# Performance work log

Hardware: AMD Instinct MI355X
Metric: run time of the kernel (lower is better)

The kernel has to match this reference:

```python
import jax, jax.numpy as jnp
import numpy as np

DIM = 256
HEADS = 8
HEAD_DIM = DIM // HEADS
SCALE = HEAD_DIM ** -0.5
EPS_LN = 1e-5
EPS_NORM = 1e-12


def setup_inputs() -> dict:
    key = jax.random.key(0)
    ks = jax.random.split(key, 12)
    B, C, H, W = 8, DIM, 32, 32
    s = 0.02
    return {
        "x": jax.random.normal(ks[0], (B, C, H, W), jnp.float32),
        "dw_w": jax.random.normal(ks[1], (C, 1, 3, 3), jnp.float32) * s,
        "dw_b": jnp.zeros((C,), jnp.float32),
        "qkv_w": jax.random.normal(ks[2], (3 * C, C), jnp.float32) * s,
        "c1_w": jax.random.normal(ks[3], (C, C), jnp.float32) * s,
        "c1_b": jnp.zeros((C,), jnp.float32),
        "ln1_g": jnp.ones((C,), jnp.float32),
        "ln1_b": jnp.zeros((C,), jnp.float32),
        "c2_w": jax.random.normal(ks[4], (C, C), jnp.float32) * s,
        "c2_b": jnp.zeros((C,), jnp.float32),
        "ln2_g": jnp.ones((C,), jnp.float32),
        "ln2_b": jnp.zeros((C,), jnp.float32),
    }


def _l2norm(t):
    n = jnp.sqrt(jnp.sum(t * t, axis=-1, keepdims=True))
    return t / jnp.maximum(n, EPS_NORM)


def _layernorm_c(x_nchw, g, b):
    # LayerNorm over channel dim of an NCHW tensor (torch does permute->LN->permute)
    mu = jnp.mean(x_nchw, axis=1, keepdims=True)
    var = jnp.mean((x_nchw - mu) ** 2, axis=1, keepdims=True)
    xn = (x_nchw - mu) * jax.lax.rsqrt(var + EPS_LN)
    return xn * g[None, :, None, None] + b[None, :, None, None]


def _gelu(x):
    return jax.nn.gelu(x, approximate=False)


def reference(x, dw_w, dw_b, qkv_w, c1_w, c1_b, ln1_g, ln1_b, c2_w, c2_b, ln2_g, ln2_b):
    B, C, H, W = x.shape
    identity = x
    # depthwise 3x3 conv
    y = jax.lax.conv_general_dilated(
        x, dw_w, window_strides=(1, 1), padding="SAME",
        dimension_numbers=("NCHW", "OIHW", "NCHW"), feature_group_count=C)
    y = y + dw_b[None, :, None, None]
    # tokens [B, N, C]
    t = y.reshape(B, C, H * W).transpose(0, 2, 1)
    qkv = jnp.einsum("bnc,oc->bno", t, qkv_w)  # [B,N,3C]
    qkv = qkv.reshape(B, H * W, 3, HEADS, HEAD_DIM).transpose(2, 0, 3, 1, 4)
    q, k, v = qkv[0], qkv[1], qkv[2]  # [B,h,N,d]
    q = _l2norm(q)
    k = _l2norm(k)
    attn = jnp.einsum("bhnd,bhmd->bhnm", q, k) * SCALE
    attn = jax.nn.softmax(attn, axis=-1)
    o = jnp.einsum("bhnm,bhmd->bhnd", attn, v)  # [B,h,N,d]
    o = o.transpose(0, 2, 1, 3).reshape(B, H * W, C)
    y = o.transpose(0, 2, 1).reshape(B, C, H, W)
    # conv-MLP branch (1x1 convs as channel GEMMs)
    y = jnp.einsum("bchw,oc->bohw", y, c1_w) + c1_b[None, :, None, None]
    y = _gelu(_layernorm_c(y, ln1_g, ln1_b))
    y = jnp.einsum("bchw,oc->bohw", y, c2_w) + c2_b[None, :, None, None]
    y = _gelu(_layernorm_c(y, ln2_g, ln2_b))
    return identity + y
```

## Files before the change

kernel.cpp:

```cpp
#include <hip/hip_runtime.h>
#include <math.h>

#define DIMC 256
#define NTOK 1024
#define QKVN 768
#define HDIM 32

typedef __attribute__((ext_vector_type(8))) short bf16x8;
typedef __attribute__((ext_vector_type(4))) float f32x4;
typedef __attribute__((ext_vector_type(4))) unsigned short us4;

__device__ __forceinline__ unsigned short f2bf(float f) {
  unsigned u = __float_as_uint(f);
  u += 0x7FFF + ((u >> 16) & 1);
  return (unsigned short)(u >> 16);
}

__device__ __forceinline__ float gelu_f(float y) {
  return 0.5f * y * (1.f + erff(y * 0.70710678118654752f));
}

__global__ void dwconv_k(const float* __restrict__ x, const float* __restrict__ w,
                         const float* __restrict__ b, float* __restrict__ y) {
  int bc = blockIdx.x;
  int c = bc & (DIMC - 1);
  float wr[9];
#pragma unroll
  for (int i = 0; i < 9; i++) wr[i] = w[c * 9 + i];
  float bb = b[c];
  const float* xp = x + (size_t)bc * NTOK;
  float* yp = y + (size_t)bc * NTOK;
  for (int p = threadIdx.x; p < NTOK; p += 256) {
    int hh = p >> 5, ww = p & 31;
    float acc = bb;
#pragma unroll
    for (int dh = 0; dh < 3; dh++) {
      int h2 = hh + dh - 1;
      if ((unsigned)h2 < 32u) {
#pragma unroll
        for (int dw = 0; dw < 3; dw++) {
          int w2 = ww + dw - 1;
          if ((unsigned)w2 < 32u) acc += xp[h2 * 32 + w2] * wr[dh * 3 + dw];
        }
      }
    }
    yp[p] = acc;
  }
}

__global__ void cvt_w_k(const float* __restrict__ w0, const float* __restrict__ w1,
                        const float* __restrict__ w2, unsigned short* __restrict__ Wb) {
  int i = (blockIdx.x * 256 + threadIdx.x) * 4;
  const float* src;
  int off;
  if (i < 196608) { src = w0; off = i; }
  else if (i < 262144) { src = w1; off = i - 196608; }
  else { src = w2; off = i - 262144; }
  float4 v = *(const float4*)(src + off);
  us4 o = {f2bf(v.x), f2bf(v.y), f2bf(v.z), f2bf(v.w)};
  *(us4*)(Wb + i) = o;
}

__global__ void t2b_k(const float* __restrict__ y2, unsigned short* __restrict__ A0) {
  __shared__ float tile[32][33];
  int b = blockIdx.z, c0 = blockIdx.y << 5, s0 = blockIdx.x << 5;
  int t = threadIdx.x;
  int j = t & 31, i0 = t >> 5;
#pragma unroll
  for (int i = i0; i < 32; i += 8)
    tile[i][j] = y2[(size_t)(b * 256 + c0 + i) * 1024 + s0 + j];
  __syncthreads();
#pragma unroll
  for (int i2 = i0; i2 < 32; i2 += 8)
    A0[(size_t)(b * 1024 + s0 + i2) * 256 + c0 + j] = f2bf(tile[j][i2]);
}

template <bool BIAS>
__global__ __launch_bounds__(256) void mgemm_k(const unsigned short* __restrict__ A,
                                               const unsigned short* __restrict__ W,
                                               const float* __restrict__ bias,
                                               float* __restrict__ C, int N) {
  __shared__ __align__(16) unsigned short As[128 * 40];
  __shared__ __align__(16) unsigned short Bs[64 * 40];
  const int t = threadIdx.x;
  const int m0 = blockIdx.y * 128;
  const int n0 = blockIdx.x * 64;
  const int wid = t >> 6, lane = t & 63;
  const int lg = lane >> 4, lr = lane & 15;
  const int wm0 = (wid >> 1) * 64, wn0 = (wid & 1) * 32;

  f32x4 acc[4][2] = {};
  for (int k0 = 0; k0 < 256; k0 += 32) {
    __syncthreads();
    {
#pragma unroll
      for (int u = 0; u < 2; u++) {
        int f = t + u * 256;
        int r = f >> 2, c = f & 3;
        bf16x8 v = *(const bf16x8*)(A + (size_t)(m0 + r) * 256 + k0 + c * 8);
        *(bf16x8*)&As[r * 40 + c * 8] = v;
      }
      int o = t >> 2, c = t & 3;
      bf16x8 v = *(const bf16x8*)(W + (size_t)(n0 + o) * 256 + k0 + c * 8);
      *(bf16x8*)&Bs[o * 40 + c * 8] = v;
    }
    __syncthreads();
    bf16x8 af[4], bfr[2];
#pragma unroll
    for (int mt = 0; mt < 4; mt++)
      af[mt] = *(const bf16x8*)&As[(wm0 + mt * 16 + lr) * 40 + lg * 8];
#pragma unroll
    for (int nt = 0; nt < 2; nt++)
      bfr[nt] = *(const bf16x8*)&Bs[(wn0 + nt * 16 + lr) * 40 + lg * 8];
#pragma unroll
    for (int mt = 0; mt < 4; mt++)
#pragma unroll
      for (int nt = 0; nt < 2; nt++)
        acc[mt][nt] = __builtin_amdgcn_mfma_f32_16x16x32_bf16(af[mt], bfr[nt], acc[mt][nt], 0, 0, 0);
  }
  float bv[2];
#pragma unroll
  for (int nt = 0; nt < 2; nt++)
    bv[nt] = BIAS ? bias[n0 + wn0 + nt * 16 + lr] : 0.f;
#pragma unroll
  for (int mt = 0; mt < 4; mt++)
#pragma unroll
    for (int nt = 0; nt < 2; nt++)
#pragma unroll
      for (int r = 0; r < 4; r++) {
        int row = m0 + wm0 + mt * 16 + lg * 4 + r;
        int col = n0 + wn0 + nt * 16 + lr;
        C[(size_t)row * N + col] = acc[mt][nt][r] + bv[nt];
      }
}

__global__ void cvt_qkv_k(const float* __restrict__ qkv,
                          unsigned short* __restrict__ Qb,
                          unsigned short* __restrict__ Kb,
                          unsigned short* __restrict__ Vb) {
  int n = blockIdx.x;
  int t = threadIdx.x;
  int b = n >> 10, nr = n & 1023;
  int sec = t >> 6, lane = t & 63;
  if (sec < 2) {
    const float* p = qkv + (size_t)n * QKVN + sec * 256 + lane * 4;
    float4 v = *(const float4*)p;
    float s = v.x * v.x + v.y * v.y + v.z * v.z + v.w * v.w;
    s += __shfl_xor(s, 1, 64); s += __shfl_xor(s, 2, 64); s += __shfl_xor(s, 4, 64);
    float inv = 1.f / fmaxf(sqrtf(s), 1e-12f);
    if (sec == 0) inv *= 0.17677669529663687f;
    int h = lane >> 3, d4 = (lane & 7) << 2;
    unsigned short* dst = (sec == 0 ? Qb : Kb) + ((size_t)((b * 8 + h) * 1024 + nr)) * 32 + d4;
    us4 o = {f2bf(v.x * inv), f2bf(v.y * inv), f2bf(v.z * inv), f2bf(v.w * inv)};
    *(us4*)dst = o;
  } else {
    int i = t - 128;
    const float* p = qkv + (size_t)n * QKVN + 512 + i * 2;
    float2 v = *(const float2*)p;
    int c = i * 2;
    int h = c >> 5, d = c & 31;
    unsigned short* dst = Vb + ((size_t)((b * 8 + h) * 1024 + nr)) * 32 + d;
    ushort2 o = {f2bf(v.x), f2bf(v.y)};
    *(ushort2*)dst = o;
  }
}

#define PSTR 56

__global__ __launch_bounds__(128) void attn_mfma_k(const unsigned short* __restrict__ Qb,
                                                   const unsigned short* __restrict__ Kb,
                                                   const unsigned short* __restrict__ Vb,
                                                   unsigned short* __restrict__ obuf) {
  __shared__ unsigned short Vt[32 * PSTR];
  __shared__ unsigned short Pl[2][32 * PSTR];
  const int bh = blockIdx.y;
  const int chunk = blockIdx.x;
  const int tid = threadIdx.x;
  const int wid = tid >> 6, lane = tid & 63;
  const int lg = lane >> 4, lr = lane & 15;
  const int q0 = chunk * 64 + wid * 32;
  const size_t base = (size_t)bh * NTOK;

  bf16x8 qf[2];
#pragma unroll
  for (int qt = 0; qt < 2; qt++)
    qf[qt] = *(const bf16x8*)(Qb + (base + q0 + qt * 16 + lr) * 32 + lg * 8);

  f32x4 o[2][2] = {};
  float lpart[2][4] = {};

  for (int step = 0; step < 32; step++) {
    const int kv0 = step * 32;
    __syncthreads();
    {
      int kv = tid >> 2, d0 = (tid & 3) * 8;
      bf16x8 v = *(const bf16x8*)(Vb + (base + kv0 + kv) * 32 + d0);
#pragma unroll
      for (int i = 0; i < 8; i++) Vt[(d0 + i) * PSTR + kv] = (unsigned short)v[i];
    }
    __syncthreads();
    bf16x8 kf[2];
#pragma unroll
    for (int ct = 0; ct < 2; ct++)
      kf[ct] = *(const bf16x8*)(Kb + (base + kv0 + ct * 16 + lr) * 32 + lg * 8);
    unsigned short* pw = &Pl[wid][0];
#pragma unroll
    for (int qt = 0; qt < 2; qt++) {
#pragma unroll
      for (int ct = 0; ct < 2; ct++) {
        f32x4 c = {};
        c = __builtin_amdgcn_mfma_f32_16x16x32_bf16(qf[qt], kf[ct], c, 0, 0, 0);
#pragma unroll
        for (int r = 0; r < 4; r++) {
          float p = __expf(c[r]);
          lpart[qt][r] += p;
          pw[(qt * 16 + lg * 4 + r) * PSTR + ct * 16 + lr] = f2bf(p);
        }
      }
    }
#pragma unroll
    for (int qt = 0; qt < 2; qt++) {
      bf16x8 pf = *(const bf16x8*)(pw + (qt * 16 + lr) * PSTR + lg * 8);
#pragma unroll
      for (int dt = 0; dt < 2; dt++) {
        bf16x8 vf = *(const bf16x8*)(&Vt[(dt * 16 + lr) * PSTR + lg * 8]);
        o[qt][dt] = __builtin_amdgcn_mfma_f32_16x16x32_bf16(pf, vf, o[qt][dt], 0, 0, 0);
      }
    }
  }
#pragma unroll
  for (int qt = 0; qt < 2; qt++) {
#pragma unroll
    for (int r = 0; r < 4; r++) {
      float l = lpart[qt][r];
      l += __shfl_xor(l, 1, 64); l += __shfl_xor(l, 2, 64);
      l += __shfl_xor(l, 4, 64); l += __shfl_xor(l, 8, 64);
      lpart[qt][r] = 1.f / l;
    }
  }
  const int b = bh >> 3, h = bh & 7;
#pragma unroll
  for (int qt = 0; qt < 2; qt++)
#pragma unroll
    for (int dt = 0; dt < 2; dt++)
#pragma unroll
      for (int r = 0; r < 4; r++) {
        int q = q0 + qt * 16 + lg * 4 + r;
        int c = h * 32 + dt * 16 + lr;
        obuf[((size_t)(b * NTOK + q)) * DIMC + c] = f2bf(o[qt][dt][r] * lpart[qt][r]);
      }
}

template <bool OBF>
__global__ void ln_gelu_k(const float* __restrict__ in, const float* __restrict__ g,
                          const float* __restrict__ bb, void* __restrict__ outv) {
  int t = threadIdx.x;
  int lane = t & 63;
  int r = blockIdx.x * 4 + (t >> 6);
  const float* p = in + ((size_t)r << 8) + (lane << 2);
  float4 v = *(const float4*)p;
  float s1 = v.x + v.y + v.z + v.w;
  float s2 = v.x * v.x + v.y * v.y + v.z * v.z + v.w * v.w;
#pragma unroll
  for (int m = 1; m < 64; m <<= 1) {
    s1 += __shfl_xor(s1, m, 64);
    s2 += __shfl_xor(s2, m, 64);
  }
  float mu = s1 * (1.f / 256.f);
  float var = s2 * (1.f / 256.f) - mu * mu;
  float rstd = rsqrtf(var + 1e-5f);
  float4 gv = *(const float4*)(g + (lane << 2));
  float4 bv = *(const float4*)(bb + (lane << 2));
  float4 ov;
  ov.x = gelu_f((v.x - mu) * rstd * gv.x + bv.x);
  ov.y = gelu_f((v.y - mu) * rstd * gv.y + bv.y);
  ov.z = gelu_f((v.z - mu) * rstd * gv.z + bv.z);
  ov.w = gelu_f((v.w - mu) * rstd * gv.w + bv.w);
  if (OBF) {
    us4 ob = {f2bf(ov.x), f2bf(ov.y), f2bf(ov.z), f2bf(ov.w)};
    *(us4*)((unsigned short*)outv + ((size_t)r << 8) + (lane << 2)) = ob;
  } else {
    *(float4*)((float*)outv + ((size_t)r << 8) + (lane << 2)) = ov;
  }
}

__global__ void trans_add_k(const float* __restrict__ m2, const float* __restrict__ x,
                            float* __restrict__ out) {
  __shared__ float tile[32][33];
  int b = blockIdx.z, c0 = blockIdx.y << 5, s0 = blockIdx.x << 5;
  int t = threadIdx.x;
  int j = t & 31, i0 = t >> 5;
#pragma unroll
  for (int i = i0; i < 32; i += 8)
    tile[i][j] = m2[(size_t)(b * 1024 + s0 + i) * 256 + c0 + j];
  __syncthreads();
#pragma unroll
  for (int i2 = i0; i2 < 32; i2 += 8) {
    size_t idx = ((size_t)(b * 256 + c0 + i2) << 10) + s0 + j;
    out[idx] = x[idx] + tile[j][i2];
  }
}

extern "C" void kernel_launch(void* const* d_in, const int* in_sizes, int n_in,
                              void* d_out, int out_size, void* d_ws, size_t ws_size,
                              hipStream_t stream) {
  const float* x     = (const float*)d_in[0];
  const float* dw_w  = (const float*)d_in[1];
  const float* dw_b  = (const float*)d_in[2];
  const float* qkv_w = (const float*)d_in[3];
  const float* c1_w  = (const float*)d_in[4];
  const float* c1_b  = (const float*)d_in[5];
  const float* ln1_g = (const float*)d_in[6];
  const float* ln1_b = (const float*)d_in[7];
  const float* c2_w  = (const float*)d_in[8];
  const float* c2_b  = (const float*)d_in[9];
  const float* ln2_g = (const float*)d_in[10];
  const float* ln2_b = (const float*)d_in[11];
  float* out = (float*)d_out;

  float* ws = (float*)d_ws;
  const size_t MF = (size_t)1 << 20;
  float* y2   = ws;
  unsigned short* A0 = (unsigned short*)(ws + 2 * MF);
  unsigned short* Wb = (unsigned short*)(ws + 3 * MF);
  float* qkv  = ws + 4 * MF;
  unsigned short* Qb = (unsigned short*)(ws + 10 * MF);
  unsigned short* Kb = (unsigned short*)(ws + 11 * MF);
  unsigned short* Vb = (unsigned short*)(ws + 12 * MF);
  unsigned short* obuf = (unsigned short*)ws;
  unsigned short* m1 = (unsigned short*)(ws + 1 * MF);
  float* buf1 = ws + 4 * MF;
  float* buf2 = ws + 6 * MF;
  float* m2b  = ws + 8 * MF;
  (void)in_sizes; (void)n_in; (void)out_size; (void)ws_size;

  dwconv_k<<<2048, 256, 0, stream>>>(x, dw_w, dw_b, y2);
  cvt_w_k<<<320, 256, 0, stream>>>(qkv_w, c1_w, c2_w, Wb);
  t2b_k<<<dim3(32, 8, 8), 256, 0, stream>>>(y2, A0);
  mgemm_k<false><<<dim3(12, 64), 256, 0, stream>>>(A0, Wb, nullptr, qkv, 768);
  cvt_qkv_k<<<8192, 256, 0, stream>>>(qkv, Qb, Kb, Vb);
  attn_mfma_k<<<dim3(16, 64), 128, 0, stream>>>(Qb, Kb, Vb, obuf);
  mgemm_k<true><<<dim3(4, 64), 256, 0, stream>>>(obuf, Wb + 196608, c1_b, buf1, 256);
  ln_gelu_k<true><<<2048, 256, 0, stream>>>(buf1, ln1_g, ln1_b, m1);
  mgemm_k<true><<<dim3(4, 64), 256, 0, stream>>>(m1, Wb + 262144, c2_b, buf2, 256);
  ln_gelu_k<false><<<2048, 256, 0, stream>>>(buf2, ln2_g, ln2_b, m2b);
  trans_add_k<<<dim3(32, 8, 8), 256, 0, stream>>>(m2b, x, out);
}
```

Baseline: 185.2 us.

## Pre-transpose V in a separate kernel and drop per-step LDS transpose in attention

Adds a kernel that writes V in a per-head transposed [d][token] bf16 layout, so the attention kernel reads V fragments straight from global memory instead of transposing into shared memory each step. The attention kernel shrinks to a single wave per block with no __syncthreads, which doubles the grid, and the P staging buffer gets a tighter stride. This removes the block barriers and LDS transpose work, but it adds one kernel launch and makes V reads uncached global accesses repeated across every query block.

```diff
diff --git a/kernel.cpp b/kernel.cpp
--- a/kernel.cpp
+++ b/kernel.cpp
@@ -136,50 +136,64 @@
 
 __global__ void cvt_qkv_k(const float* __restrict__ qkv,
                           unsigned short* __restrict__ Qb,
-                          unsigned short* __restrict__ Kb,
-                          unsigned short* __restrict__ Vb) {
+                          unsigned short* __restrict__ Kb) {
   int n = blockIdx.x;
   int t = threadIdx.x;
   int b = n >> 10, nr = n & 1023;
   int sec = t >> 6, lane = t & 63;
-  if (sec < 2) {
-    const float* p = qkv + (size_t)n * QKVN + sec * 256 + lane * 4;
-    float4 v = *(const float4*)p;
-    float s = v.x * v.x + v.y * v.y + v.z * v.z + v.w * v.w;
-    s += __shfl_xor(s, 1, 64); s += __shfl_xor(s, 2, 64); s += __shfl_xor(s, 4, 64);
-    float inv = 1.f / fmaxf(sqrtf(s), 1e-12f);
-    if (sec == 0) inv *= 0.17677669529663687f;
-    int h = lane >> 3, d4 = (lane & 7) << 2;
-    unsigned short* dst = (sec == 0 ? Qb : Kb) + ((size_t)((b * 8 + h) * 1024 + nr)) * 32 + d4;
-    us4 o = {f2bf(v.x * inv), f2bf(v.y * inv), f2bf(v.z * inv), f2bf(v.w * inv)};
-    *(us4*)dst = o;
-  } else {
-    int i = t - 128;
-    const float* p = qkv + (size_t)n * QKVN + 512 + i * 2;
-    float2 v = *(const float2*)p;
-    int c = i * 2;
-    int h = c >> 5, d = c & 31;
-    unsigned short* dst = Vb + ((size_t)((b * 8 + h) * 1024 + nr)) * 32 + d;
-    ushort2 o = {f2bf(v.x), f2bf(v.y)};
-    *(ushort2*)dst = o;
-  }
-}
-
-#define PSTR 56
-
-__global__ __launch_bounds__(128) void attn_mfma_k(const unsigned short* __restrict__ Qb,
-                                                   const unsigned short* __restrict__ Kb,
-                                                   const unsigned short* __restrict__ Vb,
-                                                   unsigned short* __restrict__ obuf) {
-  __shared__ unsigned short Vt[32 * PSTR];
-  __shared__ unsigned short Pl[2][32 * PSTR];
+  const float* p = qkv + (size_t)n * QKVN + sec * 256 + lane * 4;
+  float4 v = *(const float4*)p;
+  float s = v.x * v.x + v.y * v.y + v.z * v.z + v.w * v.w;
+  s += __shfl_xor(s, 1, 64); s += __shfl_xor(s, 2, 64); s += __shfl_xor(s, 4, 64);
+  float inv = 1.f / fmaxf(sqrtf(s), 1e-12f);
+  if (sec == 0) inv *= 0.17677669529663687f;
+  int h = lane >> 3, d4 = (lane & 7) << 2;
+  unsigned short* dst = (sec == 0 ? Qb : Kb) + ((size_t)((b * 8 + h) * 1024 + nr)) * 32 + d4;
+  us4 o = {f2bf(v.x * inv), f2bf(v.y * inv), f2bf(v.z * inv), f2bf(v.w * inv)};
+  *(us4*)dst = o;
+}
+
+#define VPAD 66
+__global__ __launch_bounds__(256) void vT_k(const float* __restrict__ qkv,
+                                            unsigned short* __restrict__ Vt) {
+  __shared__ unsigned short Vl[32 * VPAD];
+  const int tt = blockIdx.x, bh = blockIdx.y;
+  const int b = bh >> 3, h = bh & 7;
+  const int n0 = tt * 64;
+  const int t = threadIdx.x;
+  {
+    int nl = t >> 2, d8 = (t & 3) * 8;
+    const float* p = qkv + (size_t)(b * 1024 + n0 + nl) * QKVN + 512 + h * 32 + d8;
+    float4 a = *(const float4*)p;
+    float4 c = *(const float4*)(p + 4);
+    float vv[8] = {a.x, a.y, a.z, a.w, c.x, c.y, c.z, c.w};
+#pragma unroll
+    for (int i = 0; i < 8; i++) Vl[(d8 + i) * VPAD + nl] = f2bf(vv[i]);
+  }
+  __syncthreads();
+  {
+    int d = t >> 3, seg = t & 7;
+    us4 lo = *(const us4*)&Vl[d * VPAD + seg * 8];
+    us4 hi = *(const us4*)&Vl[d * VPAD + seg * 8 + 4];
+    unsigned short* dst = Vt + ((size_t)(bh * 32 + d) << 10) + n0 + seg * 8;
+    *(us4*)dst = lo;
+    *(us4*)(dst + 4) = hi;
+  }
+}
+
+#define PSTR 36
+
+__global__ __launch_bounds__(64) void attn_mfma_k(const unsigned short* __restrict__ Qb,
+                                                  const unsigned short* __restrict__ Kb,
+                                                  const unsigned short* __restrict__ Vt,
+                                                  unsigned short* __restrict__ obuf) {
+  __shared__ __align__(16) unsigned short Pl[32 * PSTR];
   const int bh = blockIdx.y;
-  const int chunk = blockIdx.x;
-  const int tid = threadIdx.x;
-  const int wid = tid >> 6, lane = tid & 63;
+  const int q0 = blockIdx.x * 32;
+  const int lane = threadIdx.x;
   const int lg = lane >> 4, lr = lane & 15;
-  const int q0 = chunk * 64 + wid * 32;
   const size_t base = (size_t)bh * NTOK;
+  const unsigned short* vb = Vt + ((size_t)bh * 32 << 10);
 
   bf16x8 qf[2];
 #pragma unroll
@@ -191,19 +205,10 @@
 
   for (int step = 0; step < 32; step++) {
     const int kv0 = step * 32;
-    __syncthreads();
-    {
-      int kv = tid >> 2, d0 = (tid & 3) * 8;
-      bf16x8 v = *(const bf16x8*)(Vb + (base + kv0 + kv) * 32 + d0);
-#pragma unroll
-      for (int i = 0; i < 8; i++) Vt[(d0 + i) * PSTR + kv] = (unsigned short)v[i];
-    }
-    __syncthreads();
     bf16x8 kf[2];
 #pragma unroll
     for (int ct = 0; ct < 2; ct++)
       kf[ct] = *(const bf16x8*)(Kb + (base + kv0 + ct * 16 + lr) * 32 + lg * 8);
-    unsigned short* pw = &Pl[wid][0];
 #pragma unroll
     for (int qt = 0; qt < 2; qt++) {
 #pragma unroll
@@ -214,16 +219,19 @@
         for (int r = 0; r < 4; r++) {
           float p = __expf(c[r]);
           lpart[qt][r] += p;
-          pw[(qt * 16 + lg * 4 + r) * PSTR + ct * 16 + lr] = f2bf(p);
+          Pl[(qt * 16 + lg * 4 + r) * PSTR + ct * 16 + lr] = f2bf(p);
         }
       }
     }
 #pragma unroll
     for (int qt = 0; qt < 2; qt++) {
-      bf16x8 pf = *(const bf16x8*)(pw + (qt * 16 + lr) * PSTR + lg * 8);
+      us4 plo = *(const us4*)&Pl[(qt * 16 + lr) * PSTR + lg * 8];
+      us4 phi = *(const us4*)&Pl[(qt * 16 + lr) * PSTR + lg * 8 + 4];
+      bf16x8 pf = {(short)plo[0], (short)plo[1], (short)plo[2], (short)plo[3],
+                   (short)phi[0], (short)phi[1], (short)phi[2], (short)phi[3]};
 #pragma unroll
       for (int dt = 0; dt < 2; dt++) {
-        bf16x8 vf = *(const bf16x8*)(&Vt[(dt * 16 + lr) * PSTR + lg * 8]);
+        bf16x8 vf = *(const bf16x8*)(vb + ((size_t)(dt * 16 + lr) << 10) + kv0 + lg * 8);
         o[qt][dt] = __builtin_amdgcn_mfma_f32_16x16x32_bf16(pf, vf, o[qt][dt], 0, 0, 0);
       }
     }
@@ -326,7 +334,7 @@
   float* qkv  = ws + 4 * MF;
   unsigned short* Qb = (unsigned short*)(ws + 10 * MF);
   unsigned short* Kb = (unsigned short*)(ws + 11 * MF);
-  unsigned short* Vb = (unsigned short*)(ws + 12 * MF);
+  unsigned short* Vtb = (unsigned short*)(ws + 12 * MF);
   unsigned short* obuf = (unsigned short*)ws;
   unsigned short* m1 = (unsigned short*)(ws + 1 * MF);
   float* buf1 = ws + 4 * MF;
@@ -338,8 +346,9 @@
   cvt_w_k<<<320, 256, 0, stream>>>(qkv_w, c1_w, c2_w, Wb);
   t2b_k<<<dim3(32, 8, 8), 256, 0, stream>>>(y2, A0);
   mgemm_k<false><<<dim3(12, 64), 256, 0, stream>>>(A0, Wb, nullptr, qkv, 768);
-  cvt_qkv_k<<<8192, 256, 0, stream>>>(qkv, Qb, Kb, Vb);
-  attn_mfma_k<<<dim3(16, 64), 128, 0, stream>>>(Qb, Kb, Vb, obuf);
+  cvt_qkv_k<<<8192, 128, 0, stream>>>(qkv, Qb, Kb);
+  vT_k<<<dim3(16, 64), 256, 0, stream>>>(qkv, Vtb);
+  attn_mfma_k<<<dim3(32, 64), 64, 0, stream>>>(Qb, Kb, Vtb, obuf);
   mgemm_k<true><<<dim3(4, 64), 256, 0, stream>>>(obuf, Wb + 196608, c1_b, buf1, 256);
   ln_gelu_k<true><<<2048, 256, 0, stream>>>(buf1, ln1_g, ln1_b, m1);
   mgemm_k<true><<<dim3(4, 64), 256, 0, stream>>>(m1, Wb + 262144, c2_b, buf2, 256);
```

Result: faster. 178.3 us (-3.7%).
